# Kernel optimization log

Measured on AMD Instinct MI355X. Metric: run time of the kernel, lower is better.

## Reference

```python
import jax, jax.numpy as jnp
import numpy as np

# DualAttention dims
D_MODEL = 1024
H_SA = 8          # self-attention heads
H_RA = 8          # relational-attention heads
TOTAL_H = H_SA + H_RA
HEAD_DIM = D_MODEL // TOTAL_H   # 64
KEY_DIM = HEAD_DIM              # 64
N_REL = 8
REL_PROJ = HEAD_DIM * H_RA // N_REL  # 64
B, S = 2, 2048


def apply_rope(x, cos, sin):
    # x: [b, s, h, d]; cos/sin: [s, d//2]. Pairs are (0,1),(2,3),... as in
    # llama-style apply_rotary_emb (reshape(..., -1, 2).unbind(-1)).
    xr, xi = x[..., 0::2], x[..., 1::2]
    c = cos[None, :, None, :]
    s_ = sin[None, :, None, :]
    out = jnp.stack([xr * c - xi * s_, xr * s_ + xi * c], axis=-1)
    return out.reshape(x.shape)


def setup_inputs() -> dict:
    key = jax.random.key(0)
    ks = jax.random.split(key, 16)
    def w(k, shape):
        return jax.random.normal(k, shape, jnp.float32) * 0.02
    x = jax.random.normal(ks[0], (B, S, D_MODEL), jnp.float32)
    symbols = jax.random.normal(ks[1], (B, S, D_MODEL), jnp.float32)
    # real RoPE tables
    pos = np.arange(S, dtype=np.float32)[:, None]
    inv = 1.0 / (10000.0 ** (np.arange(0, KEY_DIM, 2, dtype=np.float32) / KEY_DIM))
    ang = pos * inv[None, :]
    freqs_cos = jnp.asarray(np.cos(ang), jnp.float32)
    freqs_sin = jnp.asarray(np.sin(ang), jnp.float32)
    return dict(
        x=x, symbols=symbols, freqs_cos=freqs_cos, freqs_sin=freqs_sin,
        # self-attention branch (torch Linear weights: [out, in])
        wq_sa=w(ks[2], (H_SA * KEY_DIM, D_MODEL)),
        wk_sa=w(ks[3], (H_SA * KEY_DIM, D_MODEL)),
        wv_sa=w(ks[4], (H_SA * HEAD_DIM, D_MODEL)),
        wo_sa=w(ks[5], (H_SA * HEAD_DIM, H_SA * HEAD_DIM)),
        # relational-attention branch
        wq_attn=w(ks[6], (H_RA * KEY_DIM, D_MODEL)),
        wk_attn=w(ks[7], (H_RA * KEY_DIM, D_MODEL)),
        wq_rel=w(ks[8], (N_REL * REL_PROJ, D_MODEL)),
        wk_rel=w(ks[9], (N_REL * REL_PROJ, D_MODEL)),
        wr=w(ks[10], (H_RA, HEAD_DIM, N_REL)),
        wv_ra=w(ks[11], (H_RA * HEAD_DIM, D_MODEL)),
        wo_ra=w(ks[12], (H_RA * HEAD_DIM, H_RA * HEAD_DIM)),
    )


def reference(x, symbols, freqs_cos, freqs_sin,
              wq_sa, wk_sa, wv_sa, wo_sa,
              wq_attn, wk_attn, wq_rel, wk_rel, wr, wv_ra, wo_ra):
    b, s, _ = x.shape
    attn_scale = 1.0 / np.sqrt(HEAD_DIM).astype(np.float32)
    rel_scale = 1.0 / np.sqrt(REL_PROJ).astype(np.float32)
    causal = jnp.tril(jnp.ones((s, s), dtype=bool))
    neg = jnp.finfo(x.dtype).min

    def heads(t, h, d):
        return t.reshape(b, s, h, d)

    # ---- self-attention branch (causal SDPA with RoPE) ----
    q = apply_rope(heads(x @ wq_sa.T, H_SA, KEY_DIM), freqs_cos, freqs_sin)
    k = apply_rope(heads(x @ wk_sa.T, H_SA, KEY_DIM), freqs_cos, freqs_sin)
    v = heads(x @ wv_sa.T, H_SA, HEAD_DIM)
    scores = jnp.einsum('bihd,bjhd->bhij', q, k) * attn_scale
    a = jax.nn.softmax(jnp.where(causal, scores, neg), axis=-1)
    sa_out = jnp.einsum('bhij,bjhd->bihd', a, v).reshape(b, s, H_SA * HEAD_DIM) @ wo_sa.T

    # ---- relational-attention branch ----
    # attention scores (softmax selection), with RoPE
    qa = apply_rope(heads(x @ wq_attn.T, H_RA, KEY_DIM), freqs_cos, freqs_sin)
    ka = apply_rope(heads(x @ wk_attn.T, H_RA, KEY_DIM), freqs_cos, freqs_sin)
    ra_scores = jnp.einsum('bihd,bjhd->bhij', qa, ka) * attn_scale
    alpha = jax.nn.softmax(jnp.where(causal, ra_scores, neg), axis=-1)
    # relations r(x_i, x_j) in R^{N_REL} (identity rel_activation)
    qr = heads(x @ wq_rel.T, N_REL, REL_PROJ)
    kr = heads(x @ wk_rel.T, N_REL, REL_PROJ)
    rel = jnp.einsum('birp,bjrp->brij', qr, kr) * rel_scale  # [b, R, i, j]
    # symbol values: wv applied to retrieved symbols
    sv = heads(symbols @ wv_ra.T, H_RA, HEAD_DIM)
    attended_sym = jnp.einsum('bhij,bjhd->bihd', alpha, sv)          # [b, i, h, d]
    attended_rel = jnp.einsum('bhij,brij->bihr', alpha, rel)         # [b, i, h, R]
    rel_out = jnp.einsum('bihr,hdr->bihd', attended_rel, wr)
    ra_out = (attended_sym + rel_out).reshape(b, s, H_RA * HEAD_DIM) @ wo_ra.T

    # DualAttention: concat branch outputs along feature dim -> [b, s, d_model]
    return jnp.concatenate([sa_out, ra_out], axis=-1)
```

## Files before the change

kernel.cpp:

```cpp
#include <hip/hip_runtime.h>

#define B_   2
#define S_   2048
#define H_   8
#define D_   64
#define DM_  1024
#define PJ_  512
#define NT_  32
#define NTRI 528
#define NCHK 80

typedef short bf16x8 __attribute__((ext_vector_type(8)));
typedef float f32x4 __attribute__((ext_vector_type(4)));

__device__ __forceinline__ float bf2f(unsigned int u) {
  return __uint_as_float(u << 16);
}
__device__ __forceinline__ unsigned short f2bf(float f) {
  unsigned int u = __float_as_uint(f);
  u += 0x7fffu + ((u >> 16) & 1u);
  return (unsigned short)(u >> 16);
}
__device__ __forceinline__ unsigned int cvtpk_bf16(float lo, float hi) {
  unsigned int r;
  asm("v_cvt_pk_bf16_f32 %0, %1, %2" : "=v"(r) : "v"(lo), "v"(hi));
  return r;
}
__device__ __forceinline__ bf16x8 u4_to_bf(uint4 v) {
  union { uint4 a; bf16x8 b; } u; u.a = v; return u.b;
}

__device__ __forceinline__ void glds16(const unsigned short* g, unsigned short* l) {
  __builtin_amdgcn_global_load_lds(
      (const __attribute__((address_space(1))) void*)g,
      (__attribute__((address_space(3))) void*)l, 16, 0, 0);
}

struct CvtJobs {
  const float*    src[12];
  unsigned short* dst[12];
  int             n4[12];
};

__global__ __launch_bounds__(256) void cvt_many(CvtJobs J) {
  const int j = blockIdx.y;
  const int i = blockIdx.x * 256 + threadIdx.x;
  if (i >= J.n4[j]) return;
  const float4 v = ((const float4*)J.src[j])[i];
  ushort4 o;
  o.x = f2bf(v.x); o.y = f2bf(v.y); o.z = f2bf(v.z); o.w = f2bf(v.w);
  ((ushort4*)J.dst[j])[i] = o;
}

__device__ __forceinline__
void gemm128_glds(const unsigned short* __restrict__ A, int m0,
                  const unsigned short* __restrict__ Wb,
                  unsigned short* __restrict__ Cb, int ldc, int KD,
                  unsigned short* As, unsigned short* Bs)
{
  const int tid = threadIdx.x;
  const int wv = tid >> 6, lane = tid & 63;
  const int r15 = lane & 15, quad = lane >> 4;
  const int wm = (wv >> 1) * 64, wn = (wv & 1) * 64;
  f32x4 acc[4][4];
#pragma unroll
  for (int i = 0; i < 4; ++i)
#pragma unroll
    for (int j = 0; j < 4; ++j) acc[i][j] = (f32x4){0.f, 0.f, 0.f, 0.f};

  const int srow = wv * 16 + (lane >> 2);
  const int scol = ((lane & 3) ^ ((lane >> 3) & 3)) * 8;
  const unsigned short* gaA0 = A + (size_t)(m0 + srow) * KD + scol;
  const unsigned short* gaA1 = gaA0 + (size_t)64 * KD;
  const unsigned short* gaB0 = Wb + (size_t)srow * KD + scol;
  const unsigned short* gaB1 = gaB0 + (size_t)64 * KD;
  unsigned short* ldsA0 = As + wv * 512;
  unsigned short* ldsA1 = As + 2048 + wv * 512;
  unsigned short* ldsB0 = Bs + wv * 512;
  unsigned short* ldsB1 = Bs + 2048 + wv * 512;
  const int rxor = (r15 >> 1) & 3;

  for (int kk = 0; kk < KD; kk += 32) {
    __syncthreads();
    glds16(gaA0 + kk, ldsA0);
    glds16(gaA1 + kk, ldsA1);
    glds16(gaB0 + kk, ldsB0);
    glds16(gaB1 + kk, ldsB1);
    __syncthreads();
    bf16x8 af[4], bf[4];
#pragma unroll
    for (int i = 0; i < 4; ++i)
      af[i] = *(const bf16x8*)(As + (wm + i * 16 + r15) * 32 + ((quad ^ rxor) << 3));
#pragma unroll
    for (int j = 0; j < 4; ++j)
      bf[j] = *(const bf16x8*)(Bs + (wn + j * 16 + r15) * 32 + ((quad ^ rxor) << 3));
#pragma unroll
    for (int i = 0; i < 4; ++i)
#pragma unroll
      for (int j = 0; j < 4; ++j)
        acc[i][j] = __builtin_amdgcn_mfma_f32_16x16x32_bf16(af[i], bf[j], acc[i][j], 0, 0, 0);
  }
#pragma unroll
  for (int i = 0; i < 4; ++i)
#pragma unroll
    for (int r = 0; r < 4; ++r) {
      unsigned short* cp = Cb + (size_t)(wm + i * 16 + quad * 4 + r) * ldc + wn + r15;
#pragma unroll
      for (int j = 0; j < 4; ++j) cp[j * 16] = f2bf(acc[i][j][r]);
    }
}

__global__ __launch_bounds__(256)
void proj_tiled(const unsigned short* __restrict__ XB,
                const unsigned short* __restrict__ SYB,
                const unsigned short* __restrict__ Wcat,
                unsigned short* __restrict__ Qbase,
                unsigned short* __restrict__ SV)
{
  __shared__ unsigned short As[128 * 32];
  __shared__ unsigned short Bs[128 * 32];
  const int m0 = blockIdx.x * 128;
  const int ny = blockIdx.y;
  const size_t NB = (size_t)B_ * S_ * PJ_;
  const unsigned short* A;
  const unsigned short* Wb;
  unsigned short* Cb;
  if (ny < 28) {
    const int n0 = ny * 128;
    A  = XB;
    Wb = Wcat + (size_t)n0 * DM_;
    Cb = Qbase + (size_t)(n0 >> 9) * NB + (size_t)m0 * PJ_ + (n0 & 511);
  } else {
    const int n0 = (ny - 28) * 128;
    A  = SYB;
    Wb = Wcat + (size_t)7 * PJ_ * DM_ + (size_t)n0 * DM_;
    Cb = SV + (size_t)m0 * PJ_ + n0;
  }
  gemm128_glds(A, m0, Wb, Cb, PJ_, DM_, As, Bs);
}

__global__ __launch_bounds__(256)
void out_tiled(const unsigned short* __restrict__ Asa,
               const unsigned short* __restrict__ Ara,
               const unsigned short* __restrict__ WOSA,
               const unsigned short* __restrict__ WORA,
               float* __restrict__ Out)
{
  __shared__ unsigned short As[128 * 40];
  __shared__ unsigned short Bs[64 * 40];
  const int m0 = blockIdx.x * 128;
  const int ny = blockIdx.y;
  const int n0 = (ny & 7) * 64;
  const unsigned short* A  = (ny < 8) ? Asa : Ara;
  const unsigned short* Wb = ((ny < 8) ? WOSA : WORA) + (size_t)n0 * PJ_;
  float* Cb = Out + (size_t)m0 * DM_ + ((ny < 8) ? 0 : 512) + n0;

  const int tid = threadIdx.x;
  const int wv = tid >> 6, lane = tid & 63;
  const int r15 = lane & 15, quad = lane >> 4;
  const int wm = wv * 32;
  f32x4 acc[2][4];
#pragma unroll
  for (int i = 0; i < 2; ++i)
#pragma unroll
    for (int j = 0; j < 4; ++j) acc[i][j] = (f32x4){0.f, 0.f, 0.f, 0.f};

  const int arow = tid >> 1, ac = (tid & 1) * 16;
  const int brow = tid >> 2, bc = (tid & 3) * 8;
  const unsigned short* ga = A + (size_t)(m0 + arow) * PJ_ + ac;
  const unsigned short* gb = Wb + (size_t)brow * PJ_ + bc;
  unsigned short* la = As + arow * 40 + ac;
  unsigned short* lb = Bs + brow * 40 + bc;

  for (int kk = 0; kk < PJ_; kk += 32) {
    __syncthreads();
    const uint4 a0 = *(const uint4*)(ga + kk);
    const uint4 a1 = *(const uint4*)(ga + kk + 8);
    const uint4 b0 = *(const uint4*)(gb + kk);
    *(uint4*)la       = a0;
    *(uint4*)(la + 8) = a1;
    *(uint4*)lb       = b0;
    __syncthreads();
    bf16x8 af[2], bf[4];
#pragma unroll
    for (int i = 0; i < 2; ++i)
      af[i] = *(const bf16x8*)(As + (wm + i * 16 + r15) * 40 + quad * 8);
#pragma unroll
    for (int j = 0; j < 4; ++j)
      bf[j] = *(const bf16x8*)(Bs + (j * 16 + r15) * 40 + quad * 8);
#pragma unroll
    for (int i = 0; i < 2; ++i)
#pragma unroll
      for (int j = 0; j < 4; ++j)
        acc[i][j] = __builtin_amdgcn_mfma_f32_16x16x32_bf16(af[i], bf[j], acc[i][j], 0, 0, 0);
  }
#pragma unroll
  for (int i = 0; i < 2; ++i)
#pragma unroll
    for (int r = 0; r < 4; ++r) {
      float* cp = Cb + (size_t)(wm + i * 16 + quad * 4 + r) * DM_ + r15;
#pragma unroll
      for (int j = 0; j < 4; ++j) cp[j * 16] = acc[i][j][r];
    }
}

__global__ __launch_bounds__(256)
void rel_rope(const unsigned short* __restrict__ QRg, const unsigned short* __restrict__ KRg,
              unsigned short* __restrict__ RelCF,
              unsigned short* __restrict__ Qp, unsigned short* __restrict__ Kp,
              unsigned short* __restrict__ QAp, unsigned short* __restrict__ KAp,
              const float* __restrict__ fcp, const float* __restrict__ fsp)
{
  __shared__ unsigned short As[128 * 72];
  __shared__ unsigned short Bs[128 * 72];
  const int t = blockIdx.x;
  int I = 0;
  while ((I + 1) * (I + 2) / 2 <= t) ++I;
  const int J = t - I * (I + 1) / 2;
  const int rr = blockIdx.y & 7, b = blockIdx.y >> 3;
  const int tid = threadIdx.x;
  const int wv = tid >> 6, lane = tid & 63;
  const int r15 = lane & 15, quad = lane >> 4;

  const int srow = tid >> 1, c32 = (tid & 1) * 32;
  const unsigned short* ga = QRg + (size_t)(b * S_ + I * 128 + srow) * PJ_ + rr * 64 + c32;
  const unsigned short* gb = KRg + (size_t)(b * S_ + J * 128 + srow) * PJ_ + rr * 64 + c32;
  unsigned short* la = As + srow * 72 + c32;
  unsigned short* lb = Bs + srow * 72 + c32;
#pragma unroll
  for (int q = 0; q < 4; ++q) {
    *(uint4*)(la + q * 8) = *(const uint4*)(ga + q * 8);
    *(uint4*)(lb + q * 8) = *(const uint4*)(gb + q * 8);
  }
  __syncthreads();

  const int wm = (wv >> 1) * 64, wn = (wv & 1) * 64;
  const int it64 = 2 * I + (wv >> 1), jt64 = 2 * J + (wv & 1);
  if (jt64 <= it64) {
    f32x4 acc[4][4];
#pragma unroll
    for (int a = 0; a < 4; ++a)
#pragma unroll
      for (int bq = 0; bq < 4; ++bq) acc[a][bq] = (f32x4){0.f, 0.f, 0.f, 0.f};
#pragma unroll
    for (int k0 = 0; k0 < 2; ++k0) {
      bf16x8 af[4], bf[4];
#pragma unroll
      for (int i = 0; i < 4; ++i)
        af[i] = *(const bf16x8*)(As + (wm + i * 16 + r15) * 72 + quad * 8 + k0 * 32);
#pragma unroll
      for (int j = 0; j < 4; ++j)
        bf[j] = *(const bf16x8*)(Bs + (wn + j * 16 + r15) * 72 + quad * 8 + k0 * 32);
#pragma unroll
      for (int a = 0; a < 4; ++a)
#pragma unroll
        for (int bq = 0; bq < 4; ++bq)
          acc[a][bq] = __builtin_amdgcn_mfma_f32_16x16x32_bf16(bf[a], af[bq], acc[a][bq], 0, 0, 0);
    }
    unsigned short* out = RelCF + ((size_t)(b * 8 + rr) * NTRI + (size_t)it64 * (it64 + 1) / 2 + jt64) * 4096;
#pragma unroll
    for (int bq = 0; bq < 4; ++bq) {
      unsigned short tmp[16];
#pragma unroll
      for (int a = 0; a < 4; ++a)
#pragma unroll
        for (int r = 0; r < 4; ++r)
          tmp[a * 4 + r] = f2bf(acc[a][bq][r] * 0.125f);
      unsigned short* op = out + (size_t)bq * 1024 + (size_t)lane * 8;
      *(uint4*)op         = *(const uint4*)tmp;
      *(uint4*)(op + 512) = *(const uint4*)(tmp + 8);
    }
  }

  const int bid = (int)blockIdx.y * 136 + (int)blockIdx.x;
  const int gt = bid * 256 + tid;
#pragma unroll
  for (int k = 0; k < 2; ++k) {
    const int i = gt * 2 + k;
    if (i >= 4 * 262144) continue;
    const int tn = i >> 18;
    const int r2 = i & 262143;
    unsigned short* P = (tn == 0) ? Qp : (tn == 1) ? Kp : (tn == 2) ? QAp : KAp;
    const int b2 = r2 >> 17;
    const int s2 = (r2 >> 6) & 2047;
    const int c8 = (r2 & 63) * 8;
    const int ci0 = (c8 & 63) >> 1;
    const size_t off2 = ((size_t)(b2 * S_ + s2)) * PJ_ + c8;
    uint4 v = *(const uint4*)(P + off2);
    unsigned int u[4] = {v.x, v.y, v.z, v.w};
    unsigned int o[4];
#pragma unroll
    for (int q = 0; q < 4; ++q) {
      const float xr = __uint_as_float(u[q] << 16);
      const float xi = __uint_as_float(u[q] & 0xffff0000u);
      const float cs = fcp[s2 * 32 + ci0 + q];
      const float sn = fsp[s2 * 32 + ci0 + q];
      const unsigned short lo = f2bf(xr * cs - xi * sn);
      const unsigned short hi = f2bf(xr * sn + xi * cs);
      o[q] = (unsigned int)lo | ((unsigned int)hi << 16);
    }
    uint4 ov; ov.x = o[0]; ov.y = o[1]; ov.z = o[2]; ov.w = o[3];
    *(uint4*)(P + off2) = ov;
  }
}

__global__ __launch_bounds__(256)
void flash_part(const unsigned short* __restrict__ Qsa, const unsigned short* __restrict__ Ksa,
                const unsigned short* __restrict__ Vsa,
                const unsigned short* __restrict__ Qra, const unsigned short* __restrict__ Kra,
                const unsigned short* __restrict__ SVra,
                const unsigned short* __restrict__ RelCF,
                unsigned short* __restrict__ PoP, float* __restrict__ lP,
                float* __restrict__ arpP)
{
  __shared__ unsigned short Ks[2][64][72];
  __shared__ unsigned short Vt[2][64][72];
  const int x = NCHK - 1 - (int)blockIdx.x;
  int it, c;
  if (x < 8)       { it = x;                    c = 0; }
  else if (x < 24) { it = 8 + ((x - 8) >> 1);   c = (x - 8) & 1; }
  else if (x < 48) { it = 16 + (x - 24) / 3;    c = (x - 24) % 3; }
  else             { it = 24 + ((x - 48) >> 2); c = (x - 48) & 3; }
  const int j0 = c * 8;
  const int jend = (j0 + 8 < it + 1) ? (j0 + 8) : (it + 1);
  const bool ra = (blockIdx.y >= 8);
  const int h = blockIdx.y & 7;
  const int b = blockIdx.z;
  const int chunkId = (b * 16 + (int)blockIdx.y) * NCHK + x;
  const unsigned short* Qg = ra ? Qra : Qsa;
  const unsigned short* Kg = ra ? Kra : Ksa;
  const unsigned short* Vg = ra ? SVra : Vsa;
  const int tid = threadIdx.x;
  const int wv = tid >> 6, lane = tid & 63;
  const int r15 = lane & 15, quad = lane >> 4;
  const size_t bh = (size_t)b * S_ * PJ_ + (size_t)h * D_;
  const size_t relStride = (size_t)NTRI * 4096;

  const int kr0 = tid >> 3, kc0 = (tid & 7) << 3;
  const int kr1 = (tid + 256) >> 3;
  const unsigned short* kgp = Kg + bh + kc0;
  const unsigned short* vgp = Vg + bh + (size_t)lane * PJ_ + wv * 8;
  const int kcol = ((lane >> 2) & 3) * 8 + ((lane >> 4) & 1) * 4 + (lane & 3) + (lane >> 5) * 32;

  const unsigned short* qp = Qg + bh + (size_t)(it * 64 + wv * 16 + r15) * PJ_ + quad * 8;
  const bf16x8 aq0 = *(const bf16x8*)qp;
  const bf16x8 aq1 = *(const bf16x8*)(qp + 32);

  const bf16x8 ones = (bf16x8)(short)0x3F80;

  f32x4 o_acc[4];
  f32x4 l_acc = (f32x4){0.f, 0.f, 0.f, 0.f};
  f32x4 accR[8];
#pragma unroll
  for (int n = 0; n < 4; ++n) o_acc[n] = (f32x4){0.f, 0.f, 0.f, 0.f};
#pragma unroll
  for (int rr = 0; rr < 8; ++rr) accR[rr] = (f32x4){0.f, 0.f, 0.f, 0.f};
  const int il = wv * 16 + r15;
  const size_t relTileBase = (size_t)(b * 8) * NTRI * 4096
                           + (size_t)(it * (it + 1)) / 2 * 4096
                           + (size_t)wv * 1024 + (size_t)lane * 8;

  uint4 ka0, ka1, va0, va1;
  {
    const size_t jb = (size_t)j0 * 64 * PJ_;
    ka0 = *(const uint4*)(kgp + jb + (size_t)kr0 * PJ_);
    ka1 = *(const uint4*)(kgp + jb + (size_t)kr1 * PJ_);
    va0 = *(const uint4*)(vgp + jb);
    va1 = *(const uint4*)(vgp + jb + 32);
  }
  int p = 0;
  {
    *(uint4*)&Ks[0][kr0][kc0] = ka0;
    *(uint4*)&Ks[0][kr1][kc0] = ka1;
    unsigned short t8[8];
    *(uint4*)t8 = va0;
#pragma unroll
    for (int m = 0; m < 8; ++m) Vt[0][wv * 8 + m][kcol] = t8[m];
    *(uint4*)t8 = va1;
#pragma unroll
    for (int m = 0; m < 8; ++m) Vt[0][wv * 8 + 32 + m][kcol] = t8[m];
  }
  __syncthreads();

  for (int jt = j0; jt < jend; ++jt) {
    const bool more = (jt + 1 < jend);
    if (more) {
      const size_t jb = (size_t)(jt + 1) * 64 * PJ_;
      ka0 = *(const uint4*)(kgp + jb + (size_t)kr0 * PJ_);
      ka1 = *(const uint4*)(kgp + jb + (size_t)kr1 * PJ_);
      va0 = *(const uint4*)(vgp + jb);
      va1 = *(const uint4*)(vgp + jb + 32);
    }
    uint4 pre[8];
    const unsigned short* rtBase = RelCF + relTileBase + (size_t)jt * 4096;
    if (ra) {
      const unsigned short* rt = rtBase;
#pragma unroll
      for (int q = 0; q < 4; ++q) {
        pre[2 * q]     = *(const uint4*)rt;
        pre[2 * q + 1] = *(const uint4*)(rt + 512);
        rt += relStride;
      }
    }
    f32x4 s[4];
#pragma unroll
    for (int n = 0; n < 4; ++n) s[n] = (f32x4){0.f, 0.f, 0.f, 0.f};
#pragma unroll
    for (int k0 = 0; k0 < 2; ++k0) {
      const bf16x8 bq = k0 ? aq1 : aq0;
#pragma unroll
      for (int n = 0; n < 4; ++n) {
        const bf16x8 kf = *(const bf16x8*)&Ks[p][n * 16 + r15][quad * 8 + k0 * 32];
        s[n] = __builtin_amdgcn_mfma_f32_16x16x32_bf16(kf, bq, s[n], 0, 0, 0);
      }
    }
    if (jt == it) {
#pragma unroll
      for (int n = 0; n < 4; ++n)
#pragma unroll
        for (int r = 0; r < 4; ++r) {
          const bool ok = (n * 16 + quad * 4 + r <= il);
          s[n][r] = ok ? exp2f(fmaf(s[n][r], 0.180336887f, -5.770780163f)) : 0.f;
        }
    } else {
#pragma unroll
      for (int n = 0; n < 4; ++n)
#pragma unroll
        for (int r = 0; r < 4; ++r)
          s[n][r] = exp2f(fmaf(s[n][r], 0.180336887f, -5.770780163f));
    }
    uint4 w0, w1;
    w0.x = cvtpk_bf16(s[0][0], s[0][1]); w0.y = cvtpk_bf16(s[0][2], s[0][3]);
    w0.z = cvtpk_bf16(s[1][0], s[1][1]); w0.w = cvtpk_bf16(s[1][2], s[1][3]);
    w1.x = cvtpk_bf16(s[2][0], s[2][1]); w1.y = cvtpk_bf16(s[2][2], s[2][3]);
    w1.z = cvtpk_bf16(s[3][0], s[3][1]); w1.w = cvtpk_bf16(s[3][2], s[3][3]);
    const bf16x8 pa0 = u4_to_bf(w0);
    const bf16x8 pa1 = u4_to_bf(w1);
    l_acc = __builtin_amdgcn_mfma_f32_16x16x32_bf16(pa0, ones, l_acc, 0, 0, 0);
    l_acc = __builtin_amdgcn_mfma_f32_16x16x32_bf16(pa1, ones, l_acc, 0, 0, 0);
    if (ra) {
#pragma unroll
      for (int rr = 0; rr < 4; ++rr) {
        accR[rr] = __builtin_amdgcn_mfma_f32_16x16x32_bf16(pa0, u4_to_bf(pre[2 * rr]), accR[rr], 0, 0, 0);
        accR[rr] = __builtin_amdgcn_mfma_f32_16x16x32_bf16(pa1, u4_to_bf(pre[2 * rr + 1]), accR[rr], 0, 0, 0);
      }
    }
#pragma unroll
    for (int k0 = 0; k0 < 2; ++k0) {
      const bf16x8 pf = k0 ? pa1 : pa0;
#pragma unroll
      for (int n = 0; n < 4; ++n) {
        const bf16x8 vf = *(const bf16x8*)&Vt[p][n * 16 + r15][quad * 8 + k0 * 32];
        o_acc[n] = __builtin_amdgcn_mfma_f32_16x16x32_bf16(pf, vf, o_acc[n], 0, 0, 0);
      }
    }
    if (ra) {
      const unsigned short* rt2 = rtBase + 4 * relStride;
#pragma unroll
      for (int rr = 4; rr < 8; ++rr) {
        const bf16x8 rb0 = *(const bf16x8*)rt2;
        const bf16x8 rb1 = *(const bf16x8*)(rt2 + 512);
        accR[rr] = __builtin_amdgcn_mfma_f32_16x16x32_bf16(pa0, rb0, accR[rr], 0, 0, 0);
        accR[rr] = __builtin_amdgcn_mfma_f32_16x16x32_bf16(pa1, rb1, accR[rr], 0, 0, 0);
        rt2 += relStride;
      }
    }
    if (more) {
      const int q = p ^ 1;
      *(uint4*)&Ks[q][kr0][kc0] = ka0;
      *(uint4*)&Ks[q][kr1][kc0] = ka1;
      unsigned short t8[8];
      *(uint4*)t8 = va0;
#pragma unroll
      for (int m = 0; m < 8; ++m) Vt[q][wv * 8 + m][kcol] = t8[m];
      *(uint4*)t8 = va1;
#pragma unroll
      for (int m = 0; m < 8; ++m) Vt[q][wv * 8 + 32 + m][kcol] = t8[m];
      __syncthreads();
      p = q;
    }
  }
  unsigned short* po = PoP + (size_t)chunkId * 4096;
#pragma unroll
  for (int n = 0; n < 4; ++n)
#pragma unroll
    for (int r = 0; r < 4; ++r)
      po[(wv * 16 + quad * 4 + r) * 64 + n * 16 + r15] = f2bf(o_acc[n][r]);
  if (r15 == 0) {
#pragma unroll
    for (int r = 0; r < 4; ++r)
      lP[(size_t)chunkId * 64 + wv * 16 + quad * 4 + r] = l_acc[r];
  }
  if (ra && quad == (r15 >> 2)) {
    const int d3 = r15 & 3;
    float* ap = arpP + (size_t)chunkId * 512 + (size_t)(wv * 16 + r15) * 8;
#pragma unroll
    for (int rr = 0; rr < 8; ++rr) {
      const f32x4 a4 = accR[rr];
      const float v = (d3 == 0) ? a4[0] : (d3 == 1) ? a4[1] : (d3 == 2) ? a4[2] : a4[3];
      ap[rr] = v;
    }
  }
}

__global__ __launch_bounds__(256)
void flash_merge(const unsigned short* __restrict__ PoP, const float* __restrict__ lP,
                 const float* __restrict__ arpP, const float* __restrict__ wrF,
                 unsigned short* __restrict__ Osa, unsigned short* __restrict__ Ora)
{
  const int it = blockIdx.x;
  const int hh = blockIdx.y;
  const int b  = blockIdx.z;
  const bool ra = (hh >= 8);
  const int h = hh & 7;
  const int nc = it / 8 + 1;
  int cb;
  if (it < 8)       cb = it;
  else if (it < 16) cb = 8 + 2 * (it - 8);
  else if (it < 24) cb = 24 + 3 * (it - 16);
  else              cb = 48 + 4 * (it - 24);
  const int cid0 = (b * 16 + hh) * NCHK + cb;
  const int tid = threadIdx.x;
  const int row = tid >> 2;
  const int cg  = tid & 3;

  float L = 0.f;
  for (int c = 0; c < nc; ++c) L += lP[(size_t)(cid0 + c) * 64 + row];
  const float inv = 1.f / L;

  float o[16];
#pragma unroll
  for (int k = 0; k < 16; ++k) o[k] = 0.f;
  for (int c = 0; c < nc; ++c) {
    const unsigned short* pp = PoP + (size_t)(cid0 + c) * 4096 + row * 64 + cg * 16;
    unsigned int u[8];
    *(uint4*)u       = *(const uint4*)pp;
    *(uint4*)(u + 4) = *(const uint4*)(pp + 8);
#pragma unroll
    for (int q = 0; q < 8; ++q) {
      o[2 * q]     += __uint_as_float(u[q] << 16);
      o[2 * q + 1] += __uint_as_float(u[q] & 0xffff0000u);
    }
  }
  if (ra) {
    float A[8];
#pragma unroll
    for (int rr = 0; rr < 8; ++rr) A[rr] = 0.f;
    for (int c = 0; c < nc; ++c) {
      const float* ap = arpP + (size_t)(cid0 + c) * 512 + row * 8;
#pragma unroll
      for (int rr = 0; rr < 8; ++rr) A[rr] += ap[rr];
    }
#pragma unroll
    for (int k = 0; k < 16; ++k) {
      const float* wp = wrF + ((size_t)h * 64 + cg * 16 + k) * 8;
      float ro = 0.f;
#pragma unroll
      for (int rr = 0; rr < 8; ++rr) ro += A[rr] * wp[rr];
      o[k] += ro;
    }
  }
  const size_t bh = (size_t)b * S_ * PJ_ + (size_t)h * D_;
  unsigned short* op = (ra ? Ora : Osa) + bh + (size_t)(it * 64 + row) * PJ_ + cg * 16;
#pragma unroll
  for (int k = 0; k < 16; ++k) op[k] = f2bf(o[k] * inv);
}

extern "C" void kernel_launch(void* const* d_in, const int* in_sizes, int n_in,
                              void* d_out, int out_size, void* d_ws, size_t ws_size,
                              hipStream_t stream)
{
  (void)in_sizes; (void)n_in; (void)out_size; (void)ws_size;
  const float* x    = (const float*)d_in[0];
  const float* sym  = (const float*)d_in[1];
  const float* fc   = (const float*)d_in[2];
  const float* fs   = (const float*)d_in[3];
  const float* wqsa = (const float*)d_in[4];
  const float* wksa = (const float*)d_in[5];
  const float* wvsa = (const float*)d_in[6];
  const float* wosa = (const float*)d_in[7];
  const float* wqat = (const float*)d_in[8];
  const float* wkat = (const float*)d_in[9];
  const float* wqre = (const float*)d_in[10];
  const float* wkre = (const float*)d_in[11];
  const float* wr   = (const float*)d_in[12];
  const float* wvra = (const float*)d_in[13];
  const float* wora = (const float*)d_in[14];

  unsigned short* wsb = (unsigned short*)d_ws;
  const size_t NX = (size_t)B_ * S_ * DM_;
  const size_t NB = (size_t)B_ * S_ * PJ_;
  const size_t NW = (size_t)PJ_ * DM_;
  const size_t NO = (size_t)PJ_ * PJ_;
  const size_t NR = (size_t)B_ * 8 * NTRI * 4096;
  const size_t NCH = (size_t)B_ * 16 * NCHK;

  size_t off = 0;
  unsigned short* XB   = wsb + off; off += NX;
  unsigned short* SYB  = wsb + off; off += NX;
  unsigned short* WB[8];
  for (int i = 0; i < 8; ++i) { WB[i] = wsb + off; off += NW; }
  unsigned short* WOSA = wsb + off; off += NO;
  unsigned short* WORA = wsb + off; off += NO;
  unsigned short* Q    = wsb + off; off += NB;
  unsigned short* K    = wsb + off; off += NB;
  unsigned short* V    = wsb + off; off += NB;
  unsigned short* QA   = wsb + off; off += NB;
  unsigned short* KA   = wsb + off; off += NB;
  unsigned short* QR   = wsb + off; off += NB;
  unsigned short* KR   = wsb + off; off += NB;
  unsigned short* SV   = wsb + off; off += NB;
  unsigned short* Asa  = wsb + off; off += NB;
  unsigned short* Ara  = wsb + off; off += NB;
  unsigned short* RelCF = wsb + off; off += NR;
  unsigned short* PoP  = XB;
  float* lP   = (float*)(wsb + off); off += NCH * 64 * 2;
  float* arpP = (float*)(wsb + off); off += NCH * 512 * 2;

  CvtJobs cj;
  cj.src[0]  = x;    cj.dst[0]  = XB;    cj.n4[0]  = (int)(NX / 4);
  cj.src[1]  = sym;  cj.dst[1]  = SYB;   cj.n4[1]  = (int)(NX / 4);
  cj.src[2]  = wqsa; cj.dst[2]  = WB[0]; cj.n4[2]  = (int)(NW / 4);
  cj.src[3]  = wksa; cj.dst[3]  = WB[1]; cj.n4[3]  = (int)(NW / 4);
  cj.src[4]  = wvsa; cj.dst[4]  = WB[2]; cj.n4[4]  = (int)(NW / 4);
  cj.src[5]  = wqat; cj.dst[5]  = WB[3]; cj.n4[5]  = (int)(NW / 4);
  cj.src[6]  = wkat; cj.dst[6]  = WB[4]; cj.n4[6]  = (int)(NW / 4);
  cj.src[7]  = wqre; cj.dst[7]  = WB[5]; cj.n4[7]  = (int)(NW / 4);
  cj.src[8]  = wkre; cj.dst[8]  = WB[6]; cj.n4[8]  = (int)(NW / 4);
  cj.src[9]  = wvra; cj.dst[9]  = WB[7]; cj.n4[9]  = (int)(NW / 4);
  cj.src[10] = wosa; cj.dst[10] = WOSA;  cj.n4[10] = (int)(NO / 4);
  cj.src[11] = wora; cj.dst[11] = WORA;  cj.n4[11] = (int)(NO / 4);
  cvt_many<<<dim3(4096, 12), dim3(256), 0, stream>>>(cj);

  proj_tiled<<<dim3(32, 32), dim3(256), 0, stream>>>(XB, SYB, WB[0], Q, SV);
  rel_rope<<<dim3(136, 16), dim3(256), 0, stream>>>(QR, KR, RelCF, Q, K, QA, KA, fc, fs);
  flash_part<<<dim3(NCHK, 16, B_), dim3(256), 0, stream>>>(
      Q, K, V, QA, KA, SV, RelCF, PoP, lP, arpP);
  flash_merge<<<dim3(NT_, 16, B_), dim3(256), 0, stream>>>(
      PoP, lP, arpP, wr, Asa, Ara);
  out_tiled<<<dim3(32, 16), dim3(256), 0, stream>>>(Asa, Ara, WOSA, WORA, (float*)d_out);
}
```

Before: 317.7 us.

## Widen flash_part blocks to 128 query rows with paired K/V tiles

The flash partial kernel now uses 512-thread blocks that cover 128 query rows (two 64-row tiles, one per group of four waves). Each iteration stages two K/V tiles into shared memory, and causal masking and relation reads are done per wave. This halves the number of chunks and lets one staged K/V tile serve twice as many query rows, cutting global K/V traffic and chunk-scheduling overhead. The cost is more LDS per block, a larger block that may lower occupancy, some masked work on diagonal tiles, and a reworked chunk indexing in the merge kernel.

```diff
diff --git a/kernel.cpp b/kernel.cpp
--- a/kernel.cpp
+++ b/kernel.cpp
@@ -8,7 +8,7 @@
 #define PJ_  512
 #define NT_  32
 #define NTRI 528
-#define NCHK 80
+#define NCHK2 40
 
 typedef short bf16x8 __attribute__((ext_vector_type(8)));
 typedef float f32x4 __attribute__((ext_vector_type(4)));
@@ -304,7 +304,7 @@
   }
 }
 
-__global__ __launch_bounds__(256)
+__global__ __launch_bounds__(512, 4)
 void flash_part(const unsigned short* __restrict__ Qsa, const unsigned short* __restrict__ Ksa,
                 const unsigned short* __restrict__ Vsa,
                 const unsigned short* __restrict__ Qra, const unsigned short* __restrict__ Kra,
@@ -313,20 +313,21 @@
                 unsigned short* __restrict__ PoP, float* __restrict__ lP,
                 float* __restrict__ arpP)
 {
-  __shared__ unsigned short Ks[2][64][72];
-  __shared__ unsigned short Vt[2][64][72];
-  const int x = NCHK - 1 - (int)blockIdx.x;
-  int it, c;
-  if (x < 8)       { it = x;                    c = 0; }
-  else if (x < 24) { it = 8 + ((x - 8) >> 1);   c = (x - 8) & 1; }
-  else if (x < 48) { it = 16 + (x - 24) / 3;    c = (x - 24) % 3; }
-  else             { it = 24 + ((x - 48) >> 2); c = (x - 48) & 3; }
+  __shared__ unsigned short Ks[2][2][64][72];
+  __shared__ unsigned short Vt[2][2][64][72];
+  const int x = NCHK2 - 1 - (int)blockIdx.x;
+  int a, c;
+  if (x < 4)       { a = x;                 c = 0; }
+  else if (x < 12) { a = 4 + ((x - 4) >> 1);  c = (x - 4) & 1; }
+  else if (x < 24) { a = 8 + (x - 12) / 3;    c = (x - 12) % 3; }
+  else             { a = 12 + ((x - 24) >> 2); c = (x - 24) & 3; }
   const int j0 = c * 8;
-  const int jend = (j0 + 8 < it + 1) ? (j0 + 8) : (it + 1);
+  const int jendF = 2 * a + 2;
+  const int jend = (j0 + 8 < jendF) ? (j0 + 8) : jendF;
   const bool ra = (blockIdx.y >= 8);
   const int h = blockIdx.y & 7;
   const int b = blockIdx.z;
-  const int chunkId = (b * 16 + (int)blockIdx.y) * NCHK + x;
+  const int chunkId = (b * 16 + (int)blockIdx.y) * NCHK2 + x;
   const unsigned short* Qg = ra ? Qra : Qsa;
   const unsigned short* Kg = ra ? Kra : Ksa;
   const unsigned short* Vg = ra ? SVra : Vsa;
@@ -335,14 +336,15 @@
   const int r15 = lane & 15, quad = lane >> 4;
   const size_t bh = (size_t)b * S_ * PJ_ + (size_t)h * D_;
   const size_t relStride = (size_t)NTRI * 4096;
-
-  const int kr0 = tid >> 3, kc0 = (tid & 7) << 3;
-  const int kr1 = (tid + 256) >> 3;
-  const unsigned short* kgp = Kg + bh + kc0;
+  const int it_wave = 2 * a + (wv >> 2);
+  const int gi = a * 128 + wv * 16 + r15;
+
+  const int kr = tid >> 3, kc0 = (tid & 7) << 3;
+  const unsigned short* kgp = Kg + bh + (size_t)kr * PJ_ + kc0;
   const unsigned short* vgp = Vg + bh + (size_t)lane * PJ_ + wv * 8;
   const int kcol = ((lane >> 2) & 3) * 8 + ((lane >> 4) & 1) * 4 + (lane & 3) + (lane >> 5) * 32;
 
-  const unsigned short* qp = Qg + bh + (size_t)(it * 64 + wv * 16 + r15) * PJ_ + quad * 8;
+  const unsigned short* qp = Qg + bh + (size_t)gi * PJ_ + quad * 8;
   const bf16x8 aq0 = *(const bf16x8*)qp;
   const bf16x8 aq1 = *(const bf16x8*)(qp + 32);
 
@@ -355,45 +357,15 @@
   for (int n = 0; n < 4; ++n) o_acc[n] = (f32x4){0.f, 0.f, 0.f, 0.f};
 #pragma unroll
   for (int rr = 0; rr < 8; ++rr) accR[rr] = (f32x4){0.f, 0.f, 0.f, 0.f};
-  const int il = wv * 16 + r15;
   const size_t relTileBase = (size_t)(b * 8) * NTRI * 4096
-                           + (size_t)(it * (it + 1)) / 2 * 4096
-                           + (size_t)wv * 1024 + (size_t)lane * 8;
-
-  uint4 ka0, ka1, va0, va1;
-  {
-    const size_t jb = (size_t)j0 * 64 * PJ_;
-    ka0 = *(const uint4*)(kgp + jb + (size_t)kr0 * PJ_);
-    ka1 = *(const uint4*)(kgp + jb + (size_t)kr1 * PJ_);
-    va0 = *(const uint4*)(vgp + jb);
-    va1 = *(const uint4*)(vgp + jb + 32);
-  }
-  int p = 0;
-  {
-    *(uint4*)&Ks[0][kr0][kc0] = ka0;
-    *(uint4*)&Ks[0][kr1][kc0] = ka1;
-    unsigned short t8[8];
-    *(uint4*)t8 = va0;
-#pragma unroll
-    for (int m = 0; m < 8; ++m) Vt[0][wv * 8 + m][kcol] = t8[m];
-    *(uint4*)t8 = va1;
-#pragma unroll
-    for (int m = 0; m < 8; ++m) Vt[0][wv * 8 + 32 + m][kcol] = t8[m];
-  }
-  __syncthreads();
-
-  for (int jt = j0; jt < jend; ++jt) {
-    const bool more = (jt + 1 < jend);
-    if (more) {
-      const size_t jb = (size_t)(jt + 1) * 64 * PJ_;
-      ka0 = *(const uint4*)(kgp + jb + (size_t)kr0 * PJ_);
-      ka1 = *(const uint4*)(kgp + jb + (size_t)kr1 * PJ_);
-      va0 = *(const uint4*)(vgp + jb);
-      va1 = *(const uint4*)(vgp + jb + 32);
-    }
+                           + (size_t)(it_wave * (it_wave + 1)) / 2 * 4096
+                           + (size_t)(wv & 3) * 1024 + (size_t)lane * 8;
+
+  auto TILE = [&](int jtt, const unsigned short (*KsT)[72], const unsigned short (*VtT)[72]) {
+    const bool dorel = ra && (jtt <= it_wave);
+    const unsigned short* rtBase = RelCF + relTileBase + (size_t)jtt * 4096;
     uint4 pre[8];
-    const unsigned short* rtBase = RelCF + relTileBase + (size_t)jt * 4096;
-    if (ra) {
+    if (dorel) {
       const unsigned short* rt = rtBase;
 #pragma unroll
       for (int q = 0; q < 4; ++q) {
@@ -410,16 +382,16 @@
       const bf16x8 bq = k0 ? aq1 : aq0;
 #pragma unroll
       for (int n = 0; n < 4; ++n) {
-        const bf16x8 kf = *(const bf16x8*)&Ks[p][n * 16 + r15][quad * 8 + k0 * 32];
+        const bf16x8 kf = *(const bf16x8*)&KsT[n * 16 + r15][quad * 8 + k0 * 32];
         s[n] = __builtin_amdgcn_mfma_f32_16x16x32_bf16(kf, bq, s[n], 0, 0, 0);
       }
     }
-    if (jt == it) {
+    if (jtt >= it_wave) {
 #pragma unroll
       for (int n = 0; n < 4; ++n)
 #pragma unroll
         for (int r = 0; r < 4; ++r) {
-          const bool ok = (n * 16 + quad * 4 + r <= il);
+          const bool ok = (jtt * 64 + n * 16 + quad * 4 + r <= gi);
           s[n][r] = ok ? exp2f(fmaf(s[n][r], 0.180336887f, -5.770780163f)) : 0.f;
         }
     } else {
@@ -438,7 +410,7 @@
     const bf16x8 pa1 = u4_to_bf(w1);
     l_acc = __builtin_amdgcn_mfma_f32_16x16x32_bf16(pa0, ones, l_acc, 0, 0, 0);
     l_acc = __builtin_amdgcn_mfma_f32_16x16x32_bf16(pa1, ones, l_acc, 0, 0, 0);
-    if (ra) {
+    if (dorel) {
 #pragma unroll
       for (int rr = 0; rr < 4; ++rr) {
         accR[rr] = __builtin_amdgcn_mfma_f32_16x16x32_bf16(pa0, u4_to_bf(pre[2 * rr]), accR[rr], 0, 0, 0);
@@ -450,11 +422,11 @@
       const bf16x8 pf = k0 ? pa1 : pa0;
 #pragma unroll
       for (int n = 0; n < 4; ++n) {
-        const bf16x8 vf = *(const bf16x8*)&Vt[p][n * 16 + r15][quad * 8 + k0 * 32];
+        const bf16x8 vf = *(const bf16x8*)&VtT[n * 16 + r15][quad * 8 + k0 * 32];
         o_acc[n] = __builtin_amdgcn_mfma_f32_16x16x32_bf16(pf, vf, o_acc[n], 0, 0, 0);
       }
     }
-    if (ra) {
+    if (dorel) {
       const unsigned short* rt2 = rtBase + 4 * relStride;
 #pragma unroll
       for (int rr = 4; rr < 8; ++rr) {
@@ -465,22 +437,59 @@
         rt2 += relStride;
       }
     }
+  };
+
+  uint4 ka0, ka1, va0, va1;
+  {
+    const size_t jb0 = (size_t)j0 * 64 * PJ_;
+    const size_t jb1 = (size_t)(j0 + 1) * 64 * PJ_;
+    ka0 = *(const uint4*)(kgp + jb0);
+    ka1 = *(const uint4*)(kgp + jb1);
+    va0 = *(const uint4*)(vgp + jb0);
+    va1 = *(const uint4*)(vgp + jb1);
+  }
+  int p = 0;
+  {
+    *(uint4*)&Ks[0][0][kr][kc0] = ka0;
+    *(uint4*)&Ks[0][1][kr][kc0] = ka1;
+    unsigned short t8[8];
+    *(uint4*)t8 = va0;
+#pragma unroll
+    for (int m = 0; m < 8; ++m) Vt[0][0][wv * 8 + m][kcol] = t8[m];
+    *(uint4*)t8 = va1;
+#pragma unroll
+    for (int m = 0; m < 8; ++m) Vt[0][1][wv * 8 + m][kcol] = t8[m];
+  }
+  __syncthreads();
+
+  for (int jt = j0; jt < jend; jt += 2) {
+    const bool more = (jt + 2 < jend);
+    if (more) {
+      const size_t jb0 = (size_t)(jt + 2) * 64 * PJ_;
+      const size_t jb1 = (size_t)(jt + 3) * 64 * PJ_;
+      ka0 = *(const uint4*)(kgp + jb0);
+      ka1 = *(const uint4*)(kgp + jb1);
+      va0 = *(const uint4*)(vgp + jb0);
+      va1 = *(const uint4*)(vgp + jb1);
+    }
+    TILE(jt,     Ks[p][0], Vt[p][0]);
+    TILE(jt + 1, Ks[p][1], Vt[p][1]);
     if (more) {
       const int q = p ^ 1;
-      *(uint4*)&Ks[q][kr0][kc0] = ka0;
-      *(uint4*)&Ks[q][kr1][kc0] = ka1;
+      *(uint4*)&Ks[q][0][kr][kc0] = ka0;
+      *(uint4*)&Ks[q][1][kr][kc0] = ka1;
       unsigned short t8[8];
       *(uint4*)t8 = va0;
 #pragma unroll
-      for (int m = 0; m < 8; ++m) Vt[q][wv * 8 + m][kcol] = t8[m];
+      for (int m = 0; m < 8; ++m) Vt[q][0][wv * 8 + m][kcol] = t8[m];
       *(uint4*)t8 = va1;
 #pragma unroll
-      for (int m = 0; m < 8; ++m) Vt[q][wv * 8 + 32 + m][kcol] = t8[m];
+      for (int m = 0; m < 8; ++m) Vt[q][1][wv * 8 + m][kcol] = t8[m];
       __syncthreads();
       p = q;
     }
   }
-  unsigned short* po = PoP + (size_t)chunkId * 4096;
+  unsigned short* po = PoP + (size_t)chunkId * 8192;
 #pragma unroll
   for (int n = 0; n < 4; ++n)
 #pragma unroll
@@ -489,11 +498,11 @@
   if (r15 == 0) {
 #pragma unroll
     for (int r = 0; r < 4; ++r)
-      lP[(size_t)chunkId * 64 + wv * 16 + quad * 4 + r] = l_acc[r];
+      lP[(size_t)chunkId * 128 + wv * 16 + quad * 4 + r] = l_acc[r];
   }
   if (ra && quad == (r15 >> 2)) {
     const int d3 = r15 & 3;
-    float* ap = arpP + (size_t)chunkId * 512 + (size_t)(wv * 16 + r15) * 8;
+    float* ap = arpP + (size_t)chunkId * 1024 + (size_t)(wv * 16 + r15) * 8;
 #pragma unroll
     for (int rr = 0; rr < 8; ++rr) {
       const f32x4 a4 = accR[rr];
@@ -513,26 +522,29 @@
   const int b  = blockIdx.z;
   const bool ra = (hh >= 8);
   const int h = hh & 7;
-  const int nc = it / 8 + 1;
+  const int a  = it >> 1;
+  const int half = it & 1;
+  const int nc = ((2 * a + 1) >> 3) + 1;
   int cb;
-  if (it < 8)       cb = it;
-  else if (it < 16) cb = 8 + 2 * (it - 8);
-  else if (it < 24) cb = 24 + 3 * (it - 16);
-  else              cb = 48 + 4 * (it - 24);
-  const int cid0 = (b * 16 + hh) * NCHK + cb;
+  if (a < 4)       cb = a;
+  else if (a < 8)  cb = 4 + 2 * (a - 4);
+  else if (a < 12) cb = 12 + 3 * (a - 8);
+  else             cb = 24 + 4 * (a - 12);
+  const int cid0 = (b * 16 + hh) * NCHK2 + cb;
   const int tid = threadIdx.x;
   const int row = tid >> 2;
   const int cg  = tid & 3;
+  const int prow = half * 64 + row;
 
   float L = 0.f;
-  for (int c = 0; c < nc; ++c) L += lP[(size_t)(cid0 + c) * 64 + row];
+  for (int c = 0; c < nc; ++c) L += lP[(size_t)(cid0 + c) * 128 + prow];
   const float inv = 1.f / L;
 
   float o[16];
 #pragma unroll
   for (int k = 0; k < 16; ++k) o[k] = 0.f;
   for (int c = 0; c < nc; ++c) {
-    const unsigned short* pp = PoP + (size_t)(cid0 + c) * 4096 + row * 64 + cg * 16;
+    const unsigned short* pp = PoP + (size_t)(cid0 + c) * 8192 + prow * 64 + cg * 16;
     unsigned int u[8];
     *(uint4*)u       = *(const uint4*)pp;
     *(uint4*)(u + 4) = *(const uint4*)(pp + 8);
@@ -547,7 +559,7 @@
 #pragma unroll
     for (int rr = 0; rr < 8; ++rr) A[rr] = 0.f;
     for (int c = 0; c < nc; ++c) {
-      const float* ap = arpP + (size_t)(cid0 + c) * 512 + row * 8;
+      const float* ap = arpP + (size_t)(cid0 + c) * 1024 + (size_t)prow * 8;
 #pragma unroll
       for (int rr = 0; rr < 8; ++rr) A[rr] += ap[rr];
     }
@@ -593,7 +605,7 @@
   const size_t NW = (size_t)PJ_ * DM_;
   const size_t NO = (size_t)PJ_ * PJ_;
   const size_t NR = (size_t)B_ * 8 * NTRI * 4096;
-  const size_t NCH = (size_t)B_ * 16 * NCHK;
+  const size_t NCH = (size_t)B_ * 16 * NCHK2;
 
   size_t off = 0;
   unsigned short* XB   = wsb + off; off += NX;
@@ -614,8 +626,8 @@
   unsigned short* Ara  = wsb + off; off += NB;
   unsigned short* RelCF = wsb + off; off += NR;
   unsigned short* PoP  = XB;
-  float* lP   = (float*)(wsb + off); off += NCH * 64 * 2;
-  float* arpP = (float*)(wsb + off); off += NCH * 512 * 2;
+  float* lP   = (float*)(wsb + off); off += NCH * 128 * 2;
+  float* arpP = (float*)(wsb + off); off += NCH * 1024 * 2;
 
   CvtJobs cj;
   cj.src[0]  = x;    cj.dst[0]  = XB;    cj.n4[0]  = (int)(NX / 4);
@@ -634,7 +646,7 @@
 
   proj_tiled<<<dim3(32, 32), dim3(256), 0, stream>>>(XB, SYB, WB[0], Q, SV);
   rel_rope<<<dim3(136, 16), dim3(256), 0, stream>>>(QR, KR, RelCF, Q, K, QA, KA, fc, fs);
-  flash_part<<<dim3(NCHK, 16, B_), dim3(256), 0, stream>>>(
+  flash_part<<<dim3(NCHK2, 16, B_), dim3(512), 0, stream>>>(
       Q, K, V, QA, KA, SV, RelCF, PoP, lP, arpP);
   flash_merge<<<dim3(NT_, 16, B_), dim3(256), 0, stream>>>(
       PoP, lP, arpP, wr, Asa, Ara);
```

New measurement: 391.3 us. 1.23x slower.
